# Performance work log

Measured on AMD Instinct MI355X. Metric: run time of the kernel, lower is better.

The kernel has to match this reference:

```python
import jax, jax.numpy as jnp
import numpy as np

DIM = 1024
ATT_DIM = 1024
BATCH = 16384


def setup_inputs() -> dict:
    key = jax.random.key(0)
    ks = jax.random.split(key, 10)
    inp = {
        "x": jax.random.normal(ks[0], (BATCH, DIM), dtype=jnp.float32),
        "last_x": jax.random.normal(ks[1], (BATCH, DIM), dtype=jnp.float32),
        "last_num": jax.random.normal(ks[2], (BATCH, ATT_DIM), dtype=jnp.float32),
        "last_den": jax.random.uniform(ks[3], (BATCH, ATT_DIM), dtype=jnp.float32) + 1.0,
        # learned parameters
        "mix_k": jnp.full((1, DIM), 0.5, dtype=jnp.float32),
        "mix_v": jnp.full((1, DIM), 0.5, dtype=jnp.float32),
        "mix_r": jnp.full((1, DIM), 0.5, dtype=jnp.float32),
        "decay": jnp.full((1, ATT_DIM), 0.5, dtype=jnp.float32),
        "bonus": jnp.full((1, ATT_DIM), 0.5, dtype=jnp.float32),
        "Wk": jax.random.normal(ks[4], (DIM, ATT_DIM), dtype=jnp.float32) * (DIM ** -0.5),
        "Wv": jax.random.normal(ks[5], (DIM, ATT_DIM), dtype=jnp.float32) * (DIM ** -0.5),
        "Wr": jax.random.normal(ks[6], (DIM, ATT_DIM), dtype=jnp.float32) * (DIM ** -0.5),
        "Wout": jax.random.normal(ks[7], (ATT_DIM, DIM), dtype=jnp.float32) * (ATT_DIM ** -0.5),
    }
    return inp


def reference(x, last_x, last_num, last_den, mix_k, mix_v, mix_r, decay, bonus,
              Wk, Wv, Wr, Wout):
    # interpolated token-shift mixing, then thin projections
    k = (x * mix_k + last_x * (1.0 - mix_k)) @ Wk          # [B, A]
    v = (x * mix_v + last_x * (1.0 - mix_v)) @ Wv          # [B, A]
    r = jax.nn.sigmoid((x * mix_r + last_x * (1.0 - mix_r)) @ Wr)  # [B, A]

    ebk = jnp.exp(bonus + k)                                # [B, A]
    wkv = (last_num + ebk * v) / (last_den + ebk)
    rwkv = r * wkv

    w = jnp.exp(-jnp.exp(decay))                            # [1, A]
    ek = jnp.exp(k)
    num = w * last_num + ek * v
    den = w * last_den + ek

    hidden = rwkv @ Wout                                    # [B, D]
    return (hidden, x, num, den)
```

## Files before the change

kernel.cpp:

```cpp
#include <hip/hip_runtime.h>
#include <stdint.h>


typedef __bf16 bf16;
typedef __bf16 bf16x8 __attribute__((ext_vector_type(8)));
typedef float  f32x4  __attribute__((ext_vector_type(4)));

#define BATCH 16384
#define DIM   1024
#define ADIM  1024
#define FP32_MAGIC 0x3F000000u

__device__ __forceinline__ void loadbf8(const bf16* p, float* d) {
  bf16x8 a = *(const bf16x8*)p;
#pragma unroll
  for (int e = 0; e < 8; ++e) d[e] = (float)a[e];
}
__device__ __forceinline__ void storebf8(bf16* p, const float* d) {
  bf16x8 a;
#pragma unroll
  for (int e = 0; e < 8; ++e) a[e] = (bf16)d[e];
  *(bf16x8*)p = a;
}

template <typename T> struct V8;
template <> struct V8<float> {
  __device__ static void load(const float* p, float* d) {
    f32x4 a = *(const f32x4*)p; f32x4 b = *(const f32x4*)(p + 4);
#pragma unroll
    for (int e = 0; e < 4; ++e) { d[e] = a[e]; d[e + 4] = b[e]; }
  }
  __device__ static void store(float* p, const float* d) {
    f32x4 a, b;
#pragma unroll
    for (int e = 0; e < 4; ++e) { a[e] = d[e]; b[e] = d[e + 4]; }
    *(f32x4*)p = a; *(f32x4*)(p + 4) = b;
  }
};
template <> struct V8<bf16> {
  __device__ static void load(const bf16* p, float* d) { loadbf8(p, d); }
  __device__ static void store(bf16* p, const float* d) { storebf8(p, d); }
};

__device__ __forceinline__ void async_copy16(const bf16* g, bf16* l) {
  __builtin_amdgcn_global_load_lds((const __attribute__((address_space(1))) void*)g,
                                   (__attribute__((address_space(3))) void*)l,
                                   16, 0, 0);
}

template <typename TOut>
__device__ __forceinline__ void gemm_body(const bf16* A, int lda, const bf16* BT,
                                          TOut* C, bf16* As, bf16* Bs)
{
  constexpr int K = 1024, N = 1024, TK = 32;
  const int tid  = threadIdx.x;
  const int wave = tid >> 6;
  const int lane = tid & 63;
  const long m0 = (long)blockIdx.y * 128;
  const long n0 = (long)blockIdx.x * 128;
  const int wm = (wave >> 1) * 64;
  const int wn = (wave & 1) * 64;

  const int srow = lane >> 2;
  const int scol = (lane & 3) * 8;
  const bf16* gA = A  + (m0 + wave * 32 + srow) * (long)lda + scol;
  const bf16* gB = BT + (n0 + wave * 32 + srow) * (long)K   + scol;
  bf16* lA = As + (wave * 32) * TK;
  bf16* lB = Bs + (wave * 32) * TK;

  const int fr = lane & 15;
  const int fq = (lane >> 4) * 8;
  const bf16* rA = As + (wm + fr) * TK + fq;
  const bf16* rB = Bs + (wn + fr) * TK + fq;

  f32x4 acc[4][4] = {};

  for (int k0 = 0; k0 < K; k0 += TK) {
    async_copy16(gA,             lA);
    async_copy16(gA + 16 * lda,  lA + 16 * TK);
    async_copy16(gB,             lB);
    async_copy16(gB + 16 * K,    lB + 16 * TK);
    gA += TK; gB += TK;
    __syncthreads();

    bf16x8 af[4], bq[4];
#pragma unroll
    for (int t = 0; t < 4; ++t) {
      af[t] = *(const bf16x8*)(rA + t * 16 * TK);
      bq[t] = *(const bf16x8*)(rB + t * 16 * TK);
    }
#pragma unroll
    for (int i = 0; i < 4; ++i)
#pragma unroll
      for (int j = 0; j < 4; ++j)
        acc[i][j] = __builtin_amdgcn_mfma_f32_16x16x32_bf16(af[i], bq[j], acc[i][j], 0, 0, 0);
    __syncthreads();
  }

  const int cl = lane & 15;
  const int rq = (lane >> 4) * 4;
#pragma unroll
  for (int i = 0; i < 4; ++i)
#pragma unroll
    for (int j = 0; j < 4; ++j) {
      const long rowb = m0 + wm + i * 16 + rq;
      const long col  = n0 + wn + j * 16 + cl;
#pragma unroll
      for (int r = 0; r < 4; ++r)
        C[(rowb + r) * N + col] = (TOut)acc[i][j][r];
    }
}

__global__ __launch_bounds__(256) void gemm3_kernel(
    const void* outbase,
    const bf16* __restrict__ WkT, const bf16* __restrict__ WvT, const bf16* __restrict__ WrT,
    bf16* kk, bf16* vv, bf16* rp, const uint32_t* probe, long r0)
{
  __shared__ bf16 As[128 * 32];
  __shared__ bf16 Bs[128 * 32];
  const bool f32 = (*probe == FP32_MAGIC);
  const size_t es   = f32 ? 4 : 2;
  const size_t BDes = (size_t)BATCH * 1024 * es;
  const char*  base = (const char*)outbase;
  const int z = blockIdx.z;
  const size_t reg = (z == 0) ? 0 : (z == 1) ? 2 : 3;
  const bf16* A  = (const bf16*)(base + reg * BDes + (size_t)r0 * 1024 * es);
  const bf16* BT = (z == 0) ? WkT : (z == 1) ? WvT : WrT;
  bf16*       C  = (z == 0) ? kk  : (z == 1) ? vv  : rp;
  const int lda = (int)(512 * es);
  gemm_body<bf16>(A, lda, BT, C, As, Bs);
}

__global__ __launch_bounds__(256) void gemm1_kernel(
    const bf16* __restrict__ rwkv, const bf16* __restrict__ WoT,
    void* outbase, const uint32_t* probe, long r0)
{
  __shared__ bf16 As[128 * 32];
  __shared__ bf16 Bs[128 * 32];
  if (*probe == FP32_MAGIC)
    gemm_body<float>(rwkv, 1024, WoT, (float*)outbase + r0 * 1024, As, Bs);
  else
    gemm_body<bf16>(rwkv, 1024, WoT, (bf16*)outbase + r0 * 1024, As, Bs);
}

template <typename T>
__device__ __forceinline__ void transpose_body(const T* W, bf16* WT, float (*t)[33]) {
  const int tx = threadIdx.x & 31, ty = threadIdx.x >> 5;
  const int x0 = blockIdx.x * 32, y0 = blockIdx.y * 32;
#pragma unroll
  for (int i = 0; i < 32; i += 8)
    t[ty + i][tx] = (float)W[(size_t)(y0 + ty + i) * 1024 + x0 + tx];
  __syncthreads();
#pragma unroll
  for (int i = 0; i < 32; i += 8)
    WT[(size_t)(x0 + ty + i) * 1024 + y0 + tx] = (bf16)t[tx][ty + i];
}

__global__ __launch_bounds__(256) void transpose_kernel(const void* W, bf16* WT,
                                                        const uint32_t* probe) {
  __shared__ float t[32][33];
  if (*probe == FP32_MAGIC) transpose_body<float>((const float*)W, WT, t);
  else                      transpose_body<bf16>((const bf16*)W, WT, t);
}

template <typename T>
__device__ __forceinline__ void mix_body(const T* x, const T* lx,
                                         const T* mk, const T* mv, const T* mr,
                                         char* outbase)
{
  const size_t i8  = ((size_t)blockIdx.x * 256 + threadIdx.x) * 8;
  const size_t row = i8 >> 10;
  const int    col = (int)(i8 & 1023);
  constexpr size_t es = sizeof(T);
  const size_t BDes = (size_t)BATCH * 1024 * es;
  const size_t rowb = row * 1024 * es;
  bf16* xk = (bf16*)(outbase + 0 * BDes + rowb) + col;
  bf16* xv = (bf16*)(outbase + 2 * BDes + rowb) + col;
  bf16* xr = (bf16*)(outbase + 3 * BDes + rowb) + col;
  T*  xout = (T*)(outbase + 1 * BDes) + i8;

  float a[8], b[8], k[8], v[8], r[8], ok[8], ov[8], orr[8];
  V8<T>::load(x + i8, a);
  V8<T>::load(lx + i8, b);
  V8<T>::load(mk + col, k);
  V8<T>::load(mv + col, v);
  V8<T>::load(mr + col, r);
#pragma unroll
  for (int e = 0; e < 8; ++e) {
    ok[e]  = a[e] * k[e] + b[e] * (1.0f - k[e]);
    ov[e]  = a[e] * v[e] + b[e] * (1.0f - v[e]);
    orr[e] = a[e] * r[e] + b[e] * (1.0f - r[e]);
  }
  storebf8(xk, ok);
  storebf8(xv, ov);
  storebf8(xr, orr);
  V8<T>::store(xout, a);
}

__global__ __launch_bounds__(256) void mix_kernel(
    const void* x, const void* lx, const void* mk, const void* mv, const void* mr,
    void* outbase, const uint32_t* probe)
{
  if (*probe == FP32_MAGIC)
    mix_body<float>((const float*)x, (const float*)lx, (const float*)mk,
                    (const float*)mv, (const float*)mr, (char*)outbase);
  else
    mix_body<bf16>((const bf16*)x, (const bf16*)lx, (const bf16*)mk,
                   (const bf16*)mv, (const bf16*)mr, (char*)outbase);
}

template <typename T>
__device__ __forceinline__ void ew2_body(bf16* kk, const bf16* vv, const bf16* rp,
                                         const T* ln, const T* ld,
                                         const T* decay, const T* bonus,
                                         T* numo, T* deno, long grow0)
{
  const size_t li  = ((size_t)blockIdx.x * 256 + threadIdx.x) * 8;
  const size_t gi  = (size_t)grow0 + li;
  const int    col = (int)(gi & (ADIM - 1));
  float k[8], v[8], rr[8], n[8], d[8], de[8], bo[8];
  loadbf8(kk + li, k);
  loadbf8(vv + li, v);
  loadbf8(rp + li, rr);
  V8<T>::load(ln + gi, n);
  V8<T>::load(ld + gi, d);
  V8<T>::load(decay + col, de);
  V8<T>::load(bonus + col, bo);
  float orw[8], onu[8], ode[8];
#pragma unroll
  for (int e = 0; e < 8; ++e) {
    const float r   = 1.0f / (1.0f + __expf(-rr[e]));
    const float ebk = __expf(bo[e] + k[e]);
    const float wkv = (n[e] + ebk * v[e]) / (d[e] + ebk);
    orw[e] = r * wkv;
    const float w  = __expf(-__expf(de[e]));
    const float ek = __expf(k[e]);
    onu[e] = w * n[e] + ek * v[e];
    ode[e] = w * d[e] + ek;
  }
  storebf8(kk + li, orw);
  V8<T>::store(numo + gi, onu);
  V8<T>::store(deno + gi, ode);
}

__global__ __launch_bounds__(256) void ew2_kernel(
    bf16* kk, const bf16* vv, const bf16* rp,
    const void* ln, const void* ld, const void* decay, const void* bonus,
    void* outbase, const uint32_t* probe, long r0)
{
  const long grow0 = r0 * 1024;
  const long BD = (long)BATCH * 1024;
  if (*probe == FP32_MAGIC) {
    float* o = (float*)outbase;
    ew2_body<float>(kk, vv, rp, (const float*)ln, (const float*)ld,
                    (const float*)decay, (const float*)bonus,
                    o + 2 * BD, o + 3 * BD, grow0);
  } else {
    bf16* o = (bf16*)outbase;
    ew2_body<bf16>(kk, vv, rp, (const bf16*)ln, (const bf16*)ld,
                   (const bf16*)decay, (const bf16*)bonus,
                   o + 2 * BD, o + 3 * BD, grow0);
  }
}

extern "C" void kernel_launch(void* const* d_in, const int* in_sizes, int n_in,
                              void* d_out, int out_size, void* d_ws, size_t ws_size,
                              hipStream_t stream)
{
  const void* x     = d_in[0];
  const void* lx    = d_in[1];
  const void* ln    = d_in[2];
  const void* ld    = d_in[3];
  const void* mk    = d_in[4];
  const void* mv    = d_in[5];
  const void* mr    = d_in[6];
  const void* decay = d_in[7];
  const void* bonus = d_in[8];
  const void* Wk    = d_in[9];
  const void* Wv    = d_in[10];
  const void* Wr    = d_in[11];
  const void* Wo    = d_in[12];
  const uint32_t* probe = (const uint32_t*)d_in[4];

  bf16* WkT = (bf16*)d_ws;
  bf16* WvT = WkT + (size_t)DIM * ADIM;
  bf16* WrT = WvT + (size_t)DIM * ADIM;
  bf16* WoT = WrT + (size_t)DIM * ADIM;
  bf16* kk  = WoT + (size_t)DIM * ADIM;

  const size_t wt_bytes = 4ull * DIM * ADIM * sizeof(bf16);
  const size_t avail    = (ws_size > wt_bytes) ? ws_size - wt_bytes : 0;
  int chunk = BATCH;
  while (chunk > 128 && (size_t)chunk * ADIM * sizeof(bf16) * 3 > avail) chunk >>= 1;
  bf16* vv = kk + (size_t)chunk * ADIM;
  bf16* rp = vv + (size_t)chunk * ADIM;

  const dim3 tgrid(32, 32);
  transpose_kernel<<<tgrid, 256, 0, stream>>>(Wk, WkT, probe);
  transpose_kernel<<<tgrid, 256, 0, stream>>>(Wv, WvT, probe);
  transpose_kernel<<<tgrid, 256, 0, stream>>>(Wr, WrT, probe);
  transpose_kernel<<<tgrid, 256, 0, stream>>>(Wo, WoT, probe);

  mix_kernel<<<(size_t)BATCH * DIM / 2048, 256, 0, stream>>>(x, lx, mk, mv, mr,
                                                             d_out, probe);

  for (long r0 = 0; r0 < BATCH; r0 += chunk) {
    const dim3 g3(ADIM / 128, chunk / 128, 3);
    gemm3_kernel<<<g3, 256, 0, stream>>>(d_out, WkT, WvT, WrT, kk, vv, rp, probe, r0);

    ew2_kernel<<<(size_t)chunk * ADIM / 2048, 256, 0, stream>>>(
        kk, vv, rp, ln, ld, decay, bonus, d_out, probe, r0);

    const dim3 g1(DIM / 128, chunk / 128);
    gemm1_kernel<<<g1, 256, 0, stream>>>(kk , WoT, d_out, probe, r0);
  }
}
```

Before: 708.5 us.

## Rewrite GEMMs as 256x256 double-buffered swizzled-LDS MFMA pipeline

Replaces the 128x128, TK=32, single-buffered GEMM body with a 256x256 tile over 512 threads. It uses a 64-wide K step, double-buffered 128KB LDS with XOR-swizzled layout, staged async global-to-LDS loads interleaved with MFMA phases, setprio hints, and an XCD-aware tile remap. The mixed k/v/r inputs are written to a contiguous bf16 workspace when space allows, so the first GEMM reads them with a dense stride instead of from strided output regions. The aim is higher MFMA utilisation and better data reuse. The cost is much higher LDS and register pressure, and larger tiles leave fewer workgroups per kernel.

```diff
diff --git a/kernel.cpp b/kernel.cpp
--- a/kernel.cpp
+++ b/kernel.cpp
@@ -49,98 +49,201 @@
 }
 
 template <typename TOut>
-__device__ __forceinline__ void gemm_body(const bf16* A, int lda, const bf16* BT,
-                                          TOut* C, bf16* As, bf16* Bs)
-{
-  constexpr int K = 1024, N = 1024, TK = 32;
+__device__ __forceinline__ void gemm_body8(const bf16* __restrict__ A, int lda,
+                                           const bf16* __restrict__ BT,
+                                           TOut* __restrict__ C,
+                                           char* sm, int mtile, int ntile)
+{
+  constexpr int NT = 16;
   const int tid  = threadIdx.x;
   const int wave = tid >> 6;
   const int lane = tid & 63;
-  const long m0 = (long)blockIdx.y * 128;
-  const long n0 = (long)blockIdx.x * 128;
-  const int wm = (wave >> 1) * 64;
-  const int wn = (wave & 1) * 64;
-
-  const int srow = lane >> 2;
-  const int scol = (lane & 3) * 8;
-  const bf16* gA = A  + (m0 + wave * 32 + srow) * (long)lda + scol;
-  const bf16* gB = BT + (n0 + wave * 32 + srow) * (long)K   + scol;
-  bf16* lA = As + (wave * 32) * TK;
-  bf16* lB = Bs + (wave * 32) * TK;
+  const int wm = wave >> 2;
+  const int wn = wave & 3;
+  const long m0 = (long)mtile * 256;
+  const long n0 = (long)ntile * 256;
+
+  const int csrc  = (lane & 7) ^ (lane >> 3);
+  const int rbase = wave * 16 + (lane >> 3) + ((wave >= 4) ? 64 : 0);
+  const int cbase = (wave >> 1) * 64 + (wave & 1) * 16 + (lane >> 3);
+  const bf16* pA = A  + (size_t)(m0 + rbase) * lda  + csrc * 8;
+  const bf16* pB = BT + (size_t)(n0 + cbase) * 1024 + csrc * 8;
+  char* const dA = sm + wave * 2048;
+  char* const dB = sm + 32768 + wave * 2048;
 
   const int fr = lane & 15;
-  const int fq = (lane >> 4) * 8;
-  const bf16* rA = As + (wm + fr) * TK + fq;
-  const bf16* rB = Bs + (wn + fr) * TK + fq;
-
-  f32x4 acc[4][4] = {};
-
-  for (int k0 = 0; k0 < K; k0 += TK) {
-    async_copy16(gA,             lA);
-    async_copy16(gA + 16 * lda,  lA + 16 * TK);
-    async_copy16(gB,             lB);
-    async_copy16(gB + 16 * K,    lB + 16 * TK);
-    gA += TK; gB += TK;
-    __syncthreads();
-
-    bf16x8 af[4], bq[4];
-#pragma unroll
-    for (int t = 0; t < 4; ++t) {
-      af[t] = *(const bf16x8*)(rA + t * 16 * TK);
-      bq[t] = *(const bf16x8*)(rB + t * 16 * TK);
+  const int fs = lane >> 4;
+  const int c0 = ((fs ^ (fr & 7)) << 4);
+  const int c1 = (((fs ^ 4) ^ (fr & 7)) << 4);
+  const int raA = (wm * 64 + fr) * 128;
+  const int raB = 32768 + (wn * 32 + fr) * 128;
+
+  f32x4 acc[8][4] = {};
+
+#define STAGE_A(tau, u) { \
+    char* d_ = dA + (((tau) & 1) << 16) + (u) * 16384; \
+    const bf16* s_ = pA + (size_t)((u) * 64) * lda + (size_t)(tau) * 64; \
+    async_copy16(s_,           (bf16*)d_); \
+    async_copy16(s_ + 8 * lda, (bf16*)(d_ + 1024)); }
+#define STAGE_B(tau, u) { \
+    char* d_ = dB + (((tau) & 1) << 16) + (u) * 16384; \
+    const bf16* s_ = pB + (size_t)((u) * 32) * 1024 + (size_t)(tau) * 64; \
+    async_copy16(s_,            (bf16*)d_); \
+    async_copy16(s_ + 8 * 1024, (bf16*)(d_ + 1024)); }
+
+  STAGE_B(0, 0); STAGE_A(0, 0); STAGE_A(0, 1); STAGE_B(0, 1);
+  STAGE_B(1, 0); STAGE_A(1, 0);
+  asm volatile("s_waitcnt vmcnt(4)" ::: "memory");
+  __builtin_amdgcn_s_barrier();
+  __builtin_amdgcn_sched_barrier(0);
+
+#pragma unroll 2
+  for (int t = 0; t < NT; ++t) {
+    char* const sb = sm + ((t & 1) << 16);
+    bf16x8 a0[4][2], a1[4][2], bq[2][2];
+
+#pragma unroll
+    for (int mf = 0; mf < 4; ++mf) {
+      a0[mf][0] = *(const bf16x8*)(sb + raA + mf * 2048 + c0);
+      a0[mf][1] = *(const bf16x8*)(sb + raA + mf * 2048 + c1);
     }
 #pragma unroll
-    for (int i = 0; i < 4; ++i)
-#pragma unroll
-      for (int j = 0; j < 4; ++j)
-        acc[i][j] = __builtin_amdgcn_mfma_f32_16x16x32_bf16(af[i], bq[j], acc[i][j], 0, 0, 0);
-    __syncthreads();
-  }
-
-  const int cl = lane & 15;
-  const int rq = (lane >> 4) * 4;
-#pragma unroll
-  for (int i = 0; i < 4; ++i)
-#pragma unroll
-    for (int j = 0; j < 4; ++j) {
-      const long rowb = m0 + wm + i * 16 + rq;
-      const long col  = n0 + wn + j * 16 + cl;
+    for (int nf = 0; nf < 2; ++nf) {
+      bq[nf][0] = *(const bf16x8*)(sb + raB + nf * 2048 + c0);
+      bq[nf][1] = *(const bf16x8*)(sb + raB + nf * 2048 + c1);
+    }
+    if (t + 1 < NT) STAGE_A(t + 1, 1);
+    __builtin_amdgcn_s_barrier();
+    asm volatile("s_waitcnt lgkmcnt(0)" ::: "memory");
+    __builtin_amdgcn_s_setprio(1);
+#pragma unroll
+    for (int kk = 0; kk < 2; ++kk)
+#pragma unroll
+      for (int mf = 0; mf < 4; ++mf)
+#pragma unroll
+        for (int nf = 0; nf < 2; ++nf)
+          acc[mf][nf] = __builtin_amdgcn_mfma_f32_16x16x32_bf16(
+              a0[mf][kk], bq[nf][kk], acc[mf][nf], 0, 0, 0);
+    __builtin_amdgcn_s_setprio(0);
+    __builtin_amdgcn_s_barrier();
+
+#pragma unroll
+    for (int mf = 0; mf < 4; ++mf) {
+      a1[mf][0] = *(const bf16x8*)(sb + raA + 16384 + mf * 2048 + c0);
+      a1[mf][1] = *(const bf16x8*)(sb + raA + 16384 + mf * 2048 + c1);
+    }
+    if (t + 1 < NT) STAGE_B(t + 1, 1);
+    __builtin_amdgcn_s_barrier();
+    asm volatile("s_waitcnt lgkmcnt(0)" ::: "memory");
+    __builtin_amdgcn_s_setprio(1);
+#pragma unroll
+    for (int kk = 0; kk < 2; ++kk)
+#pragma unroll
+      for (int mf = 0; mf < 4; ++mf)
+#pragma unroll
+        for (int nf = 0; nf < 2; ++nf)
+          acc[4 + mf][nf] = __builtin_amdgcn_mfma_f32_16x16x32_bf16(
+              a1[mf][kk], bq[nf][kk], acc[4 + mf][nf], 0, 0, 0);
+    __builtin_amdgcn_s_setprio(0);
+    __builtin_amdgcn_s_barrier();
+
+#pragma unroll
+    for (int nf = 0; nf < 2; ++nf) {
+      bq[nf][0] = *(const bf16x8*)(sb + raB + 16384 + nf * 2048 + c0);
+      bq[nf][1] = *(const bf16x8*)(sb + raB + 16384 + nf * 2048 + c1);
+    }
+    if (t + 2 < NT) STAGE_B(t + 2, 0);
+    __builtin_amdgcn_s_barrier();
+    asm volatile("s_waitcnt lgkmcnt(0)" ::: "memory");
+    __builtin_amdgcn_s_setprio(1);
+#pragma unroll
+    for (int kk = 0; kk < 2; ++kk)
+#pragma unroll
+      for (int mf = 0; mf < 4; ++mf)
+#pragma unroll
+        for (int nf = 0; nf < 2; ++nf)
+          acc[mf][2 + nf] = __builtin_amdgcn_mfma_f32_16x16x32_bf16(
+              a0[mf][kk], bq[nf][kk], acc[mf][2 + nf], 0, 0, 0);
+    __builtin_amdgcn_s_setprio(0);
+    __builtin_amdgcn_s_barrier();
+
+    if (t + 2 < NT) STAGE_A(t + 2, 0);
+    __builtin_amdgcn_s_setprio(1);
+#pragma unroll
+    for (int kk = 0; kk < 2; ++kk)
+#pragma unroll
+      for (int mf = 0; mf < 4; ++mf)
+#pragma unroll
+        for (int nf = 0; nf < 2; ++nf)
+          acc[4 + mf][2 + nf] = __builtin_amdgcn_mfma_f32_16x16x32_bf16(
+              a1[mf][kk], bq[nf][kk], acc[4 + mf][2 + nf], 0, 0, 0);
+    __builtin_amdgcn_s_setprio(0);
+    if (t < NT - 2)       { asm volatile("s_waitcnt vmcnt(4)" ::: "memory"); }
+    else if (t == NT - 2) { asm volatile("s_waitcnt vmcnt(0)" ::: "memory"); }
+    __builtin_amdgcn_s_barrier();
+    __builtin_amdgcn_sched_barrier(0);
+  }
+#undef STAGE_A
+#undef STAGE_B
+
+  const int cl = fr, rq = fs * 4;
+#pragma unroll
+  for (int mf = 0; mf < 8; ++mf)
+#pragma unroll
+    for (int nf = 0; nf < 4; ++nf) {
+      const size_t rb = (size_t)(m0 + wm * 128 + mf * 16 + rq) * 1024
+                      + (size_t)(n0 + wn * 64 + nf * 16 + cl);
 #pragma unroll
       for (int r = 0; r < 4; ++r)
-        C[(rowb + r) * N + col] = (TOut)acc[i][j][r];
+        C[rb + (size_t)r * 1024] = (TOut)acc[mf][nf][r];
     }
 }
 
-__global__ __launch_bounds__(256) void gemm3_kernel(
-    const void* outbase,
+__device__ __forceinline__ void swz_tiles(int& mtile, int& ntile) {
+  const int nbx = gridDim.x, nwg = gridDim.x * gridDim.y;
+  int flat = blockIdx.x + blockIdx.y * nbx;
+  if ((nwg & 7) == 0 && nwg >= 16) {
+    const int cpx = nwg >> 3;
+    flat = (flat & 7) * cpx + (flat >> 3);
+  }
+  ntile = flat % nbx; mtile = flat / nbx;
+}
+
+__global__ __launch_bounds__(512, 2) void gemm3_kernel(
+    const void* outbase, const bf16* __restrict__ xs,
     const bf16* __restrict__ WkT, const bf16* __restrict__ WvT, const bf16* __restrict__ WrT,
     bf16* kk, bf16* vv, bf16* rp, const uint32_t* probe, long r0)
 {
-  __shared__ bf16 As[128 * 32];
-  __shared__ bf16 Bs[128 * 32];
-  const bool f32 = (*probe == FP32_MAGIC);
-  const size_t es   = f32 ? 4 : 2;
-  const size_t BDes = (size_t)BATCH * 1024 * es;
-  const char*  base = (const char*)outbase;
+  __shared__ char sm[131072];
+  int mtile, ntile; swz_tiles(mtile, ntile);
   const int z = blockIdx.z;
-  const size_t reg = (z == 0) ? 0 : (z == 1) ? 2 : 3;
-  const bf16* A  = (const bf16*)(base + reg * BDes + (size_t)r0 * 1024 * es);
   const bf16* BT = (z == 0) ? WkT : (z == 1) ? WvT : WrT;
-  bf16*       C  = (z == 0) ? kk  : (z == 1) ? vv  : rp;
-  const int lda = (int)(512 * es);
-  gemm_body<bf16>(A, lda, BT, C, As, Bs);
-}
-
-__global__ __launch_bounds__(256) void gemm1_kernel(
+  bf16*       Cz = (z == 0) ? kk  : (z == 1) ? vv  : rp;
+  const bf16* Az; int lda;
+  if (xs) {
+    Az  = xs + (size_t)z * BATCH * 1024 + (size_t)r0 * 1024;
+    lda = 1024;
+  } else {
+    const bool f32 = (*probe == FP32_MAGIC);
+    const size_t es = f32 ? 4 : 2;
+    const size_t reg = (z == 0) ? 0 : (z == 1) ? 2 : 3;
+    Az  = (const bf16*)((const char*)outbase + reg * (size_t)BATCH * 1024 * es
+                        + (size_t)r0 * 1024 * es);
+    lda = (int)(512 * es);
+  }
+  gemm_body8<bf16>(Az, lda, BT, Cz, sm, mtile, ntile);
+}
+
+__global__ __launch_bounds__(512, 2) void gemm1_kernel(
     const bf16* __restrict__ rwkv, const bf16* __restrict__ WoT,
     void* outbase, const uint32_t* probe, long r0)
 {
-  __shared__ bf16 As[128 * 32];
-  __shared__ bf16 Bs[128 * 32];
+  __shared__ char sm[131072];
+  int mtile, ntile; swz_tiles(mtile, ntile);
   if (*probe == FP32_MAGIC)
-    gemm_body<float>(rwkv, 1024, WoT, (float*)outbase + r0 * 1024, As, Bs);
+    gemm_body8<float>(rwkv, 1024, WoT, (float*)outbase + (size_t)r0 * 1024, sm, mtile, ntile);
   else
-    gemm_body<bf16>(rwkv, 1024, WoT, (bf16*)outbase + r0 * 1024, As, Bs);
+    gemm_body8<bf16>(rwkv, 1024, WoT, (bf16*)outbase + (size_t)r0 * 1024, sm, mtile, ntile);
 }
 
 template <typename T>
@@ -166,18 +269,24 @@
 template <typename T>
 __device__ __forceinline__ void mix_body(const T* x, const T* lx,
                                          const T* mk, const T* mv, const T* mr,
-                                         char* outbase)
+                                         char* outbase, bf16* xs)
 {
   const size_t i8  = ((size_t)blockIdx.x * 256 + threadIdx.x) * 8;
   const size_t row = i8 >> 10;
   const int    col = (int)(i8 & 1023);
   constexpr size_t es = sizeof(T);
   const size_t BDes = (size_t)BATCH * 1024 * es;
-  const size_t rowb = row * 1024 * es;
-  bf16* xk = (bf16*)(outbase + 0 * BDes + rowb) + col;
-  bf16* xv = (bf16*)(outbase + 2 * BDes + rowb) + col;
-  bf16* xr = (bf16*)(outbase + 3 * BDes + rowb) + col;
-  T*  xout = (T*)(outbase + 1 * BDes) + i8;
+  bf16 *xk, *xv, *xr;
+  if (xs) {
+    const size_t BD = (size_t)BATCH * 1024;
+    xk = xs + i8; xv = xs + BD + i8; xr = xs + 2 * BD + i8;
+  } else {
+    const size_t rowb = row * 1024 * es;
+    xk = (bf16*)(outbase + 0 * BDes + rowb) + col;
+    xv = (bf16*)(outbase + 2 * BDes + rowb) + col;
+    xr = (bf16*)(outbase + 3 * BDes + rowb) + col;
+  }
+  T* xout = (T*)(outbase + 1 * BDes) + i8;
 
   float a[8], b[8], k[8], v[8], r[8], ok[8], ov[8], orr[8];
   V8<T>::load(x + i8, a);
@@ -199,14 +308,14 @@
 
 __global__ __launch_bounds__(256) void mix_kernel(
     const void* x, const void* lx, const void* mk, const void* mv, const void* mr,
-    void* outbase, const uint32_t* probe)
+    void* outbase, bf16* xs, const uint32_t* probe)
 {
   if (*probe == FP32_MAGIC)
     mix_body<float>((const float*)x, (const float*)lx, (const float*)mk,
-                    (const float*)mv, (const float*)mr, (char*)outbase);
+                    (const float*)mv, (const float*)mr, (char*)outbase, xs);
   else
     mix_body<bf16>((const bf16*)x, (const bf16*)lx, (const bf16*)mk,
-                   (const bf16*)mv, (const bf16*)mr, (char*)outbase);
+                   (const bf16*)mv, (const bf16*)mr, (char*)outbase, xs);
 }
 
 template <typename T>
@@ -286,12 +395,24 @@
   bf16* WvT = WkT + (size_t)DIM * ADIM;
   bf16* WrT = WvT + (size_t)DIM * ADIM;
   bf16* WoT = WrT + (size_t)DIM * ADIM;
-  bf16* kk  = WoT + (size_t)DIM * ADIM;
 
   const size_t wt_bytes = 4ull * DIM * ADIM * sizeof(bf16);
-  const size_t avail    = (ws_size > wt_bytes) ? ws_size - wt_bytes : 0;
-  int chunk = BATCH;
-  while (chunk > 128 && (size_t)chunk * ADIM * sizeof(bf16) * 3 > avail) chunk >>= 1;
+  const size_t xs_bytes = 3ull * BATCH * DIM * sizeof(bf16);
+  const size_t kv_bytes = 3ull * BATCH * ADIM * sizeof(bf16);
+
+  bf16* xs = nullptr;
+  bf16* kk;
+  int chunk;
+  if (ws_size >= wt_bytes + xs_bytes + kv_bytes) {
+    xs = WoT + (size_t)DIM * ADIM;
+    kk = xs + 3ull * BATCH * DIM;
+    chunk = BATCH;
+  } else {
+    kk = WoT + (size_t)DIM * ADIM;
+    const size_t avail = (ws_size > wt_bytes) ? ws_size - wt_bytes : 0;
+    chunk = BATCH;
+    while (chunk > 256 && (size_t)chunk * ADIM * sizeof(bf16) * 3 > avail) chunk >>= 1;
+  }
   bf16* vv = kk + (size_t)chunk * ADIM;
   bf16* rp = vv + (size_t)chunk * ADIM;
 
@@ -302,16 +423,16 @@
   transpose_kernel<<<tgrid, 256, 0, stream>>>(Wo, WoT, probe);
 
   mix_kernel<<<(size_t)BATCH * DIM / 2048, 256, 0, stream>>>(x, lx, mk, mv, mr,
-                                                             d_out, probe);
+                                                             d_out, xs, probe);
 
   for (long r0 = 0; r0 < BATCH; r0 += chunk) {
-    const dim3 g3(ADIM / 128, chunk / 128, 3);
-    gemm3_kernel<<<g3, 256, 0, stream>>>(d_out, WkT, WvT, WrT, kk, vv, rp, probe, r0);
+    const dim3 g3(ADIM / 256, chunk / 256, 3);
+    gemm3_kernel<<<g3, 512, 0, stream>>>(d_out, xs, WkT, WvT, WrT, kk, vv, rp, probe, r0);
 
     ew2_kernel<<<(size_t)chunk * ADIM / 2048, 256, 0, stream>>>(
         kk, vv, rp, ln, ld, decay, bonus, d_out, probe, r0);
 
-    const dim3 g1(DIM / 128, chunk / 128);
-    gemm1_kernel<<<g1, 256, 0, stream>>>(kk , WoT, d_out, probe, r0);
-  }
-}
+    const dim3 g1(DIM / 256, chunk / 256);
+    gemm1_kernel<<<g1, 512, 0, stream>>>(kk , WoT, d_out, probe, r0);
+  }
+}
```

Measured after the change: 646.3 us. 8.8% less time.
